# Optimization experiments

Measured on AMD Instinct MI355X. Metric: run time of the kernel, lower is better.

## Reference

```python
import jax, jax.numpy as jnp
import numpy as np

B, LE, LD = 8, 4096, 4096
DE, DD, A = 512, 512, 128


def setup_inputs() -> dict:
    key = jax.random.key(0)
    ks = jax.random.split(key, 9)
    f32 = jnp.float32
    return {
        "encoder_outputs": jax.random.normal(ks[0], (B, LE, DE), f32),
        "decoder_outputs": jax.random.normal(ks[1], (B, LD, DD), f32),
        # linear_q / linear_k / linear_v (Dense with bias, relu activation)
        "Wq": jax.random.normal(ks[2], (DD, A), f32) * 0.05,
        "bq": jnp.zeros((A,), f32),
        "Wk": jax.random.normal(ks[3], (DE, A), f32) * 0.05,
        "bk": jnp.zeros((A,), f32),
        "Wv": jax.random.normal(ks[4], (DE, A), f32) * 0.05,
        "bv": jnp.zeros((A,), f32),
        # perceptron branch weights (Dense, no bias)
        "Pw": jax.random.normal(ks[5], (A, A), f32) * 0.05,
        "Pu": jax.random.normal(ks[6], (A, A), f32) * 0.05,
        "pv": jax.random.normal(ks[7], (A, 1), f32) * 0.05,
    }


def reference(encoder_outputs, decoder_outputs, Wq, bq, Wk, bk, Wv, bv, Pw, Pu, pv):
    att = Wq.shape[1]
    q = jax.nn.relu(decoder_outputs @ Wq + bq)   # [B, Ld, A]
    k = jax.nn.relu(encoder_outputs @ Wk + bk)   # [B, Le, A]
    v = jax.nn.relu(encoder_outputs @ Wv + bv)   # [B, Le, A]
    # perceptron score: pv^T (Pw q_i + Pu k_j). No nonlinearity between the
    # sum and pv, so it decomposes additively -> no [B,Ld,Le,A] tiling needed.
    q_term = (q @ Pw) @ pv                        # [B, Ld, 1]
    k_term = (k @ Pu) @ pv                        # [B, Le, 1]
    scores = (q_term + jnp.swapaxes(k_term, 1, 2)) / jnp.sqrt(jnp.float32(att))  # [B, Ld, Le]
    weights = jax.nn.softmax(scores, axis=-1)
    attention = jnp.einsum('bij,bjd->bid', weights, v)  # [B, Ld, A]
    return attention
```

## Files before the change

kernel.cpp:

```cpp
#include <hip/hip_runtime.h>
#include <hip/hip_bf16.h>

#define B_   8
#define KDIM 512
#define AA_  128
#define RTOT 32768
#define NDIM 256

typedef __attribute__((ext_vector_type(8))) short short8;
typedef __attribute__((ext_vector_type(4))) float f32x4;

#define WCT_OFF   0
#define U_OFF     262144
#define BIAS_OFF  262656
#define PARTS_OFF 263680
#define S_OFF     296448
#define VB_OFF    427520

__device__ inline ushort f2bf(float f) {
    union { float f; unsigned u; } x; x.f = f;
    unsigned r = x.u + 0x7fffu + ((x.u >> 16) & 1u);
    return (ushort)(r >> 16);
}
__device__ inline float bf2f(ushort s) {
    union { unsigned u; float f; } x; x.u = ((unsigned)s) << 16;
    return x.f;
}

__global__ void prep_kernel(const float* __restrict__ Wk, const float* __restrict__ bk,
                            const float* __restrict__ Wv, const float* __restrict__ bv,
                            const float* __restrict__ Pu, const float* __restrict__ pv,
                            ushort* __restrict__ wct, float* __restrict__ u,
                            float* __restrict__ bias) {
    int t = threadIdx.x;
    int base = blockIdx.x * 256 + t;
    for (int i = 0; i < 4; ++i) {
        int idx = base + i * 32768;
        int n = idx >> 9, k = idx & 511;
        float s = (n < 128) ? Wk[k * 128 + n] : Wv[k * 128 + (n - 128)];
        wct[idx] = f2bf(s);
    }
    if (blockIdx.x == 0) {
        if (t < 128) {
            float acc = 0.f;
            for (int c = 0; c < 128; ++c) acc += Pu[t * 128 + c] * pv[c];
            u[t] = acc;
        }
        bias[t] = (t < 128) ? bk[t] : bv[t - 128];
    }
}

__global__ __launch_bounds__(512, 4)
void gemm_fused(const float* __restrict__ enc, const ushort* __restrict__ wct,
                const float* __restrict__ bias, const float* __restrict__ u,
                ushort* __restrict__ vbuf, float* __restrict__ sout) {
    __shared__ ushort As[64][72];
    __shared__ ushort Bs[256][72];
    __shared__ float s_red[64][2];
    const int t = threadIdx.x;
    const int wv = t >> 6, l = t & 63;
    const int wm = wv >> 2, wn = wv & 3;
    const int m = l & 15, kb = l >> 4;
    const int row0 = blockIdx.x * 64;

    const int ar = t >> 3, ak8 = (t & 7) * 8;
    const float* aptr = enc + (size_t)(row0 + ar) * KDIM + ak8;

    f32x4 acc[2][4] = {};
    float4 a0, a1;
    int4 bp[4];

    a0 = *(const float4*)aptr;
    a1 = *(const float4*)(aptr + 4);
#pragma unroll
    for (int i = 0; i < 4; ++i) {
        int c = t + i * 512, n = c >> 3, k8 = (c & 7) * 8;
        bp[i] = *(const int4*)(wct + (size_t)n * KDIM + k8);
    }

    for (int st = 0; st < 8; ++st) {
        {
            int4 pk;
            pk.x = (int)f2bf(a0.x) | ((int)f2bf(a0.y) << 16);
            pk.y = (int)f2bf(a0.z) | ((int)f2bf(a0.w) << 16);
            pk.z = (int)f2bf(a1.x) | ((int)f2bf(a1.y) << 16);
            pk.w = (int)f2bf(a1.z) | ((int)f2bf(a1.w) << 16);
            *(int4*)&As[ar][ak8] = pk;
#pragma unroll
            for (int i = 0; i < 4; ++i) {
                int c = t + i * 512, n = c >> 3, k8 = (c & 7) * 8;
                *(int4*)&Bs[n][k8] = bp[i];
            }
        }
        __syncthreads();
        if (st < 7) {
            const float* ap = aptr + (st + 1) * 64;
            a0 = *(const float4*)ap;
            a1 = *(const float4*)(ap + 4);
#pragma unroll
            for (int i = 0; i < 4; ++i) {
                int c = t + i * 512, n = c >> 3, k8 = (c & 7) * 8;
                bp[i] = *(const int4*)(wct + (size_t)n * KDIM + (st + 1) * 64 + k8);
            }
        }
#pragma unroll
        for (int kc = 0; kc < 2; ++kc) {
            short8 afr[2], bfr[4];
#pragma unroll
            for (int mt = 0; mt < 2; ++mt)
                afr[mt] = *(const short8*)&As[wm * 32 + mt * 16 + m][kc * 32 + kb * 8];
#pragma unroll
            for (int nt = 0; nt < 4; ++nt)
                bfr[nt] = *(const short8*)&Bs[wn * 64 + nt * 16 + m][kc * 32 + kb * 8];
#pragma unroll
            for (int mt = 0; mt < 2; ++mt)
#pragma unroll
                for (int nt = 0; nt < 4; ++nt)
                    acc[mt][nt] = __builtin_amdgcn_mfma_f32_16x16x32_bf16(
                        afr[mt], bfr[nt], acc[mt][nt], 0, 0, 0);
        }
        __syncthreads();
    }

    const int rg = kb;
    if (wn < 2) {
#pragma unroll
        for (int mt = 0; mt < 2; ++mt) {
            float p[4] = {0.f, 0.f, 0.f, 0.f};
#pragma unroll
            for (int nt = 0; nt < 4; ++nt) {
                int col = wn * 64 + nt * 16 + m;
                float bsv = bias[col], uw = u[col];
#pragma unroll
                for (int j = 0; j < 4; ++j) {
                    float vvv = acc[mt][nt][j] + bsv;
                    vvv = vvv > 0.f ? vvv : 0.f;
                    p[j] += vvv * uw;
                }
            }
#pragma unroll
            for (int j = 0; j < 4; ++j) {
                p[j] += __shfl_xor(p[j], 1);
                p[j] += __shfl_xor(p[j], 2);
                p[j] += __shfl_xor(p[j], 4);
                p[j] += __shfl_xor(p[j], 8);
            }
            if (m == 0) {
#pragma unroll
                for (int j = 0; j < 4; ++j)
                    s_red[wm * 32 + mt * 16 + rg * 4 + j][wn] = p[j];
            }
        }
    } else {
#pragma unroll
        for (int mt = 0; mt < 2; ++mt) {
#pragma unroll
            for (int nt = 0; nt < 4; ++nt) {
                int col = wn * 64 + nt * 16 + m;
                float bsv = bias[col];
#pragma unroll
                for (int j = 0; j < 4; ++j) {
                    int rowl = wm * 32 + mt * 16 + rg * 4 + j;
                    float vvv = acc[mt][nt][j] + bsv;
                    vvv = vvv > 0.f ? vvv : 0.f;
                    vbuf[(size_t)(row0 + rowl) * AA_ + (col - 128)] = f2bf(vvv);
                }
            }
        }
    }
    __syncthreads();
    if (t < 64) sout[row0 + t] = s_red[t][0] + s_red[t][1];
}

__global__ __launch_bounds__(256)
void wsum_kernel(const ushort* __restrict__ vbuf, const float* __restrict__ sg,
                 float* __restrict__ parts) {
    __shared__ float redM[5], redS[5];
    __shared__ float pw[4][128];
    const int blk = blockIdx.x;
    const int b = blk >> 3, ch = blk & 7;
    const int t = threadIdx.x, wv = t >> 6, l = t & 63;
    const float inv_s = 0.08838834764831843f;

    float vl[16], mx = -1e30f;
#pragma unroll
    for (int i = 0; i < 16; ++i) {
        vl[i] = sg[b * 4096 + i * 256 + t];
        mx = fmaxf(mx, vl[i]);
    }
#pragma unroll
    for (int off = 1; off < 64; off <<= 1) mx = fmaxf(mx, __shfl_xor(mx, off));
    if (l == 0) redM[wv] = mx;
    __syncthreads();
    if (t == 0) redM[4] = fmaxf(fmaxf(redM[0], redM[1]), fmaxf(redM[2], redM[3]));
    __syncthreads();
    const float M = redM[4];
    float sm = 0.f;
#pragma unroll
    for (int i = 0; i < 16; ++i) sm += __expf((vl[i] - M) * inv_s);
#pragma unroll
    for (int off = 1; off < 64; off <<= 1) sm += __shfl_xor(sm, off);
    if (l == 0) redS[wv] = sm;
    __syncthreads();
    if (t == 0) redS[4] = 1.0f / (redS[0] + redS[1] + redS[2] + redS[3]);
    __syncthreads();
    const float rS = redS[4];

    const int rg = l >> 4, d8 = (l & 15) * 8;
    const int rbase = b * 4096 + ch * 512;
    float acc[8] = {};
    for (int it = 0; it < 32; ++it) {
        int r = rbase + it * 16 + wv * 4 + rg;
        float wj = __expf((sg[r] - M) * inv_s) * rS;
        short8 vvv = *(const short8*)(vbuf + (size_t)r * AA_ + d8);
#pragma unroll
        for (int j = 0; j < 8; ++j)
            acc[j] += wj * bf2f((ushort)vvv[j]);
    }
#pragma unroll
    for (int j = 0; j < 8; ++j) {
        acc[j] += __shfl_xor(acc[j], 16);
        acc[j] += __shfl_xor(acc[j], 32);
    }
    if (l < 16) {
#pragma unroll
        for (int j = 0; j < 8; ++j) pw[wv][d8 + j] = acc[j];
    }
    __syncthreads();
    if (t < 128) parts[blk * 128 + t] = pw[0][t] + pw[1][t] + pw[2][t] + pw[3][t];
}

__global__ __launch_bounds__(256)
void bcast_kernel(const float* __restrict__ parts, float4* __restrict__ out) {
    __shared__ float4 nv[32];
    const int t = threadIdx.x;
    const int c = blockIdx.x * 256 + t;
    const int b = (blockIdx.x * 1024) >> 19;
    if (t < 32) {
        const float4* p4 = (const float4*)parts;
        float4 s = {0.f, 0.f, 0.f, 0.f};
#pragma unroll
        for (int ch = 0; ch < 8; ++ch) {
            float4 q = p4[(b * 8 + ch) * 32 + t];
            s.x += q.x; s.y += q.y; s.z += q.z; s.w += q.w;
        }
        nv[t] = s;
    }
    __syncthreads();
    out[c] = nv[t & 31];
}

extern "C" void kernel_launch(void* const* d_in, const int* in_sizes, int n_in,
                              void* d_out, int out_size, void* d_ws, size_t ws_size,
                              hipStream_t stream) {
    const float* enc = (const float*)d_in[0];
    const float* Wk = (const float*)d_in[4];
    const float* bk = (const float*)d_in[5];
    const float* Wv = (const float*)d_in[6];
    const float* bv = (const float*)d_in[7];
    const float* Pu = (const float*)d_in[9];
    const float* pv = (const float*)d_in[10];

    char* ws = (char*)d_ws;
    ushort* wct   = (ushort*)(ws + WCT_OFF);
    float*  u     = (float*)(ws + U_OFF);
    float*  bias  = (float*)(ws + BIAS_OFF);
    float*  parts = (float*)(ws + PARTS_OFF);
    float*  sg    = (float*)(ws + S_OFF);
    ushort* vbuf  = (ushort*)(ws + VB_OFF);

    prep_kernel<<<128, 256, 0, stream>>>(Wk, bk, Wv, bv, Pu, pv, wct, u, bias);
    gemm_fused<<<RTOT / 64, 512, 0, stream>>>(enc, wct, bias, u, vbuf, sg);
    wsum_kernel<<<64, 256, 0, stream>>>(vbuf, sg, parts);
    bcast_kernel<<<4096, 256, 0, stream>>>(parts, (float4*)d_out);
}
```

Baseline: 214.3 us.

## Halve GEMM row tile and stream weight tiles directly into LDS

The fused K/V projection GEMM now uses 32-row tiles with 256-thread blocks, doubling the grid. The weight tile is copied straight from global memory into shared memory with global_load_lds, replacing the register prefetch and the separate LDS store. The aim is to cut register pressure and per-block staging work, and to improve occupancy and load balance. The costs are twice as much total weight traffic (mostly from L2), no prefetch overlap for the weight tile, and an unpadded shared B layout that may cause bank conflicts on the MFMA fragment reads.

```diff
diff --git a/kernel.cpp b/kernel.cpp
--- a/kernel.cpp
+++ b/kernel.cpp
@@ -5,7 +5,8 @@
 #define KDIM 512
 #define AA_  128
 #define RTOT 32768
-#define NDIM 256
+#define BM   32
+#define NGRID (RTOT/BM)
 
 typedef __attribute__((ext_vector_type(8))) short short8;
 typedef __attribute__((ext_vector_type(4))) float f32x4;
@@ -25,6 +26,12 @@
 __device__ inline float bf2f(ushort s) {
     union { unsigned u; float f; } x; x.u = ((unsigned)s) << 16;
     return x.f;
+}
+
+__device__ __forceinline__ void glds16(const void* g, void* l) {
+    __builtin_amdgcn_global_load_lds(
+        (const __attribute__((address_space(1))) void*)g,
+        (__attribute__((address_space(3))) void*)l, 16, 0, 0);
 }
 
 __global__ void prep_kernel(const float* __restrict__ Wk, const float* __restrict__ bk,
@@ -50,68 +57,63 @@
     }
 }
 
-__global__ __launch_bounds__(512, 4)
+__global__ __launch_bounds__(256, 4)
 void gemm_fused(const float* __restrict__ enc, const ushort* __restrict__ wct,
                 const float* __restrict__ bias, const float* __restrict__ u,
                 ushort* __restrict__ vbuf, float* __restrict__ sout) {
-    __shared__ ushort As[64][72];
-    __shared__ ushort Bs[256][72];
-    __shared__ float s_red[64][2];
+    __shared__ ushort As[BM][72];
+    __shared__ ushort Bs[256][64];
+    __shared__ float s_red[BM][2];
     const int t = threadIdx.x;
     const int wv = t >> 6, l = t & 63;
-    const int wm = wv >> 2, wn = wv & 3;
     const int m = l & 15, kb = l >> 4;
-    const int row0 = blockIdx.x * 64;
+    const int rg = kb;
+    const int row0 = blockIdx.x * BM;
 
     const int ar = t >> 3, ak8 = (t & 7) * 8;
     const float* aptr = enc + (size_t)(row0 + ar) * KDIM + ak8;
 
+    const int brow = (l >> 3);
+    const int bcolB = (l & 7) << 4;
+
     f32x4 acc[2][4] = {};
     float4 a0, a1;
-    int4 bp[4];
 
     a0 = *(const float4*)aptr;
     a1 = *(const float4*)(aptr + 4);
-#pragma unroll
-    for (int i = 0; i < 4; ++i) {
-        int c = t + i * 512, n = c >> 3, k8 = (c & 7) * 8;
-        bp[i] = *(const int4*)(wct + (size_t)n * KDIM + k8);
-    }
 
     for (int st = 0; st < 8; ++st) {
         {
+            const char* gbase = (const char*)wct + (size_t)st * 128 + bcolB;
+#pragma unroll
+            for (int i = 0; i < 8; ++i) {
+                int c = (wv << 3) | i;
+                int row = (c << 3) + brow;
+                glds16(gbase + (size_t)row * 1024,
+                       (char*)Bs + c * 1024 + l * 16);
+            }
             int4 pk;
             pk.x = (int)f2bf(a0.x) | ((int)f2bf(a0.y) << 16);
             pk.y = (int)f2bf(a0.z) | ((int)f2bf(a0.w) << 16);
             pk.z = (int)f2bf(a1.x) | ((int)f2bf(a1.y) << 16);
             pk.w = (int)f2bf(a1.z) | ((int)f2bf(a1.w) << 16);
             *(int4*)&As[ar][ak8] = pk;
-#pragma unroll
-            for (int i = 0; i < 4; ++i) {
-                int c = t + i * 512, n = c >> 3, k8 = (c & 7) * 8;
-                *(int4*)&Bs[n][k8] = bp[i];
-            }
         }
         __syncthreads();
         if (st < 7) {
             const float* ap = aptr + (st + 1) * 64;
             a0 = *(const float4*)ap;
             a1 = *(const float4*)(ap + 4);
-#pragma unroll
-            for (int i = 0; i < 4; ++i) {
-                int c = t + i * 512, n = c >> 3, k8 = (c & 7) * 8;
-                bp[i] = *(const int4*)(wct + (size_t)n * KDIM + (st + 1) * 64 + k8);
-            }
         }
 #pragma unroll
         for (int kc = 0; kc < 2; ++kc) {
             short8 afr[2], bfr[4];
 #pragma unroll
             for (int mt = 0; mt < 2; ++mt)
-                afr[mt] = *(const short8*)&As[wm * 32 + mt * 16 + m][kc * 32 + kb * 8];
+                afr[mt] = *(const short8*)&As[mt * 16 + m][kc * 32 + kb * 8];
 #pragma unroll
             for (int nt = 0; nt < 4; ++nt)
-                bfr[nt] = *(const short8*)&Bs[wn * 64 + nt * 16 + m][kc * 32 + kb * 8];
+                bfr[nt] = *(const short8*)&Bs[wv * 64 + nt * 16 + m][kc * 32 + kb * 8];
 #pragma unroll
             for (int mt = 0; mt < 2; ++mt)
 #pragma unroll
@@ -122,14 +124,13 @@
         __syncthreads();
     }
 
-    const int rg = kb;
-    if (wn < 2) {
+    if (wv < 2) {
 #pragma unroll
         for (int mt = 0; mt < 2; ++mt) {
             float p[4] = {0.f, 0.f, 0.f, 0.f};
 #pragma unroll
             for (int nt = 0; nt < 4; ++nt) {
-                int col = wn * 64 + nt * 16 + m;
+                int col = wv * 64 + nt * 16 + m;
                 float bsv = bias[col], uw = u[col];
 #pragma unroll
                 for (int j = 0; j < 4; ++j) {
@@ -148,7 +149,7 @@
             if (m == 0) {
 #pragma unroll
                 for (int j = 0; j < 4; ++j)
-                    s_red[wm * 32 + mt * 16 + rg * 4 + j][wn] = p[j];
+                    s_red[mt * 16 + rg * 4 + j][wv] = p[j];
             }
         }
     } else {
@@ -156,11 +157,11 @@
         for (int mt = 0; mt < 2; ++mt) {
 #pragma unroll
             for (int nt = 0; nt < 4; ++nt) {
-                int col = wn * 64 + nt * 16 + m;
+                int col = wv * 64 + nt * 16 + m;
                 float bsv = bias[col];
 #pragma unroll
                 for (int j = 0; j < 4; ++j) {
-                    int rowl = wm * 32 + mt * 16 + rg * 4 + j;
+                    int rowl = mt * 16 + rg * 4 + j;
                     float vvv = acc[mt][nt][j] + bsv;
                     vvv = vvv > 0.f ? vvv : 0.f;
                     vbuf[(size_t)(row0 + rowl) * AA_ + (col - 128)] = f2bf(vvv);
@@ -169,7 +170,7 @@
         }
     }
     __syncthreads();
-    if (t < 64) sout[row0 + t] = s_red[t][0] + s_red[t][1];
+    if (t < BM) sout[row0 + t] = s_red[t][0] + s_red[t][1];
 }
 
 __global__ __launch_bounds__(256)
@@ -270,7 +271,7 @@
     ushort* vbuf  = (ushort*)(ws + VB_OFF);
 
     prep_kernel<<<128, 256, 0, stream>>>(Wk, bk, Wv, bv, Pu, pv, wct, u, bias);
-    gemm_fused<<<RTOT / 64, 512, 0, stream>>>(enc, wct, bias, u, vbuf, sg);
+    gemm_fused<<<NGRID, 256, 0, stream>>>(enc, wct, bias, u, vbuf, sg);
     wsum_kernel<<<64, 256, 0, stream>>>(vbuf, sg, parts);
     bcast_kernel<<<4096, 256, 0, stream>>>(parts, (float4*)d_out);
 }
```

New measurement: 181.4 us. -15.4%, faster.
